# Kernel tuning notes

Measured on AMD Instinct MI355X. Metric: run time of the kernel, lower is better.

The kernel has to match this reference:

```python
import jax, jax.numpy as jnp
import numpy as np
from functools import reduce

N_QUBITS = 12
DIM = 2 ** N_QUBITS          # 4096 state-vector dimension
DEPTH = 6                    # ansatz rotation layers
BATCH = 256
OBSERVE_BITS = (0, 1, 2)     # Pauli-Z expectation on these qubits
INPUT_SCALING = np.pi


def setup_inputs() -> dict:
    key = jax.random.key(0)
    k1, k2 = jax.random.split(key)
    input_tensor = jax.random.uniform(k1, (BATCH, N_QUBITS), dtype=jnp.float32)
    # param_init_range = (-pi/depth, pi/depth)
    thetas = jax.random.normal(k2, (DEPTH, N_QUBITS), dtype=jnp.float32) * (np.pi / DEPTH)
    return {"input_tensor": input_tensor, "thetas": thetas}


def _ry(theta):
    # RY(theta) = [[cos t/2, -sin t/2], [sin t/2, cos t/2]]
    h = theta * 0.5
    c, s = jnp.cos(h), jnp.sin(h)
    return jnp.stack([jnp.stack([c, -s]), jnp.stack([s, c])]).astype(jnp.complex64)


def _cnot_ladder_perm():
    # CNOT(i -> i+1) for i = 0..n-2; each CNOT is a basis permutation that
    # flips the target bit when the control bit is 1. Compose permutations
    # (applied in reverse order so state_out = state_in[perm]). Qubit 0 is the
    # leftmost kron factor, i.e. bit position n-1-q of the basis index.
    perm = np.arange(DIM)
    for cq, tq in reversed([(i, i + 1) for i in range(N_QUBITS - 1)]):
        cbit, tbit = N_QUBITS - 1 - cq, N_QUBITS - 1 - tq
        flip = ((perm >> cbit) & 1) == 1
        perm = np.where(flip, perm ^ (1 << tbit), perm)
    return jnp.asarray(perm)


_PERM = _cnot_ladder_perm()


def _forward(input_tensor, thetas):
    # --- encoder: RY(pi * x_q) applied to |0...0> gives a product state ---
    half = input_tensor * (INPUT_SCALING * 0.5)          # [B, n] half-angles
    c, s = jnp.cos(half), jnp.sin(half)
    psi = jnp.ones((BATCH, 1), dtype=jnp.complex64)
    for q in range(N_QUBITS):                            # fixed small loop over qubits
        amp = jnp.stack([c[:, q], s[:, q]], axis=-1).astype(jnp.complex64)  # [B, 2]
        psi = (psi[:, :, None] * amp[:, None, :]).reshape(BATCH, -1)
    state = psi.T                                        # [DIM, B] complex64

    # --- ansatz: per-depth full-unitary (kron of per-qubit gates) mm, then CNOT ladder ---
    for d in range(DEPTH):
        U = reduce(jnp.kron, [_ry(thetas[d, q]) for q in range(N_QUBITS)])  # [DIM, DIM]
        state = U @ state                                # Hamiltonian @ state (torch.mm)
        state = state[_PERM]                             # entangling CNOT ladder

    # --- observer: <Z_q> on each observed qubit ---
    probs = state.real ** 2 + state.imag ** 2            # [DIM, B]
    idx = jnp.arange(DIM)
    zdiag = jnp.stack([1.0 - 2.0 * ((idx >> (N_QUBITS - 1 - q)) & 1)
                       for q in OBSERVE_BITS]).astype(jnp.float32)          # [K, DIM]
    return jnp.einsum('kn,nb->bk', zdiag, probs)         # [B, K]


def reference(input_tensor, thetas):
    return _forward(input_tensor, thetas)
```

## Files before the change

### kernel.cpp

```cpp
#include <hip/hip_runtime.h>
#include <math.h>
#include <type_traits>

#define NQ     12
#define DIM    4096
#define DEPTH  6
#define NBATCH 256
#define NT     256
#define NREG   16


__host__ __device__ constexpr unsigned axmask(int d, int b) {
    unsigned m = 1u << b;
    for (int i = 0; i < d; ++i) m = (m ^ (m >> 1)) & 0xFFFu;
    return m;
}
__host__ __device__ constexpr unsigned selmask(int d, int b) {
    unsigned m = 1u << b;
    for (int i = 0; i < 16 - d; ++i) m = (m ^ ((m << 1) & 0xFFFu)) & 0xFFFu;
    return m;
}
__host__ __device__ constexpr int cpopc(unsigned v) {
    int c = 0; while (v) { c += (int)(v & 1u); v >>= 1; } return c;
}

template<int I, int N, class F>
__device__ __forceinline__ void sfor(F&& f) {
    if constexpr (I < N) {
        f(std::integral_constant<int, I>{});
        sfor<I + 1, N>(static_cast<F&&>(f));
    }
}

template<int CTRL>
__device__ __forceinline__ float dppx(float v) {
    int iv = __float_as_int(v);
    return __int_as_float(__builtin_amdgcn_update_dpp(iv, iv, CTRL, 0xF, 0xF, false));
}
template<int M4>
__device__ __forceinline__ float lxor_low(float v) {
    static_assert(M4 >= 1 && M4 <= 15, "low mask");
    if constexpr      (M4 == 1)  return dppx<0xB1>(v);
    else if constexpr (M4 == 2)  return dppx<0x4E>(v);
    else if constexpr (M4 == 3)  return dppx<0x1B>(v);
    else if constexpr (M4 == 7)  return dppx<0x141>(v);
    else if constexpr (M4 == 15) return dppx<0x140>(v);
    else if constexpr ((M4 & 8) == 0)
        return lxor_low<M4 ^ 7>(dppx<0x141>(v));
    else
        return lxor_low<M4 ^ 15>(dppx<0x140>(v));
}
template<int MASK>
__device__ __forceinline__ float lxor(float v) {
    static_assert(MASK > 0 && MASK < 64, "lane mask");
    if constexpr (MASK >= 32) {
        return __shfl_xor(v, MASK, 64);
    } else if constexpr (MASK >= 16) {
        return __int_as_float(__builtin_amdgcn_ds_swizzle(__float_as_int(v),
                                                          (MASK << 10) | 0x1F));
    } else {
        return lxor_low<MASK>(v);
    }
}

template<int D, int B>
__device__ __forceinline__ void gate_reg(float (&st)[NREG], int tid, float t) {
    constexpr unsigned V = axmask(D, B), M = selmask(D, B);
    static_assert((V >> 4) == 0 && V != 0, "reg gate");
    constexpr int VR = (int)V;
    constexpr unsigned MR = M & 15u, MT = M >> 4;
    const float tp = (__popc(MT & (unsigned)tid) & 1) ? t : -t;
    const float tn = -tp;
    sfor<0, NREG>([&](auto RC) {
        constexpr int r = RC.value, r2 = r ^ VR;
        if constexpr (r2 > r) {
            constexpr bool p0 = (cpopc(MR & (unsigned)r)  & 1) != 0;
            constexpr bool p1 = (cpopc(MR & (unsigned)r2) & 1) != 0;
            float a0 = st[r];
            st[r]  = fmaf(p0 ? tn : tp, st[r2], st[r]);
            st[r2] = fmaf(p1 ? tn : tp, a0,     st[r2]);
        }
    });
}

template<int D, int B>
__device__ __forceinline__ void gate_lane(float (&st)[NREG], int tid, float t) {
    constexpr unsigned V = axmask(D, B), M = selmask(D, B);
    constexpr int VT = (int)(V >> 4), VR = (int)(V & 15u);
    static_assert(VT > 0 && VT < 64, "intra-wave gate");
    static_assert((M & 15u) == 0, "no reg bits in selector for b>=4");
    const float tp = (__popc((M >> 4) & (unsigned)tid) & 1) ? t : -t;
    if constexpr (VR == 0) {
        sfor<0, NREG>([&](auto RC) {
            constexpr int r = RC.value;
            float p = lxor<VT>(st[r]);
            st[r] = fmaf(tp, p, st[r]);
        });
    } else {
        sfor<0, NREG>([&](auto RC) {
            constexpr int r = RC.value, r2 = r ^ VR;
            if constexpr (r2 > r) {
                float pa = lxor<VT>(st[r2]);
                float pb = lxor<VT>(st[r]);
                st[r]  = fmaf(tp, pa, st[r]);
                st[r2] = fmaf(tp, pb, st[r2]);
            }
        });
    }
}

template<int D>
__device__ __forceinline__ void cross2(float (&st)[NREG], int tid,
                                       float t1, float t2,
                                       float* __restrict__ lds) {
    constexpr unsigned V1 = axmask(D, 11), V2 = axmask(D, 10);
    constexpr unsigned M1 = selmask(D, 11), M2 = selmask(D, 10);
    static_assert((V1 & 15u) == 0 && (V2 & 15u) == 0, "cross axes thread-pure");
    static_assert((M1 & 15u) == 0 && (M2 & 15u) == 0, "cross masks thread-pure");
    constexpr int T1 = (int)(V1 >> 4), T2 = (int)(V2 >> 4);
    static_assert((cpopc(M1 & V2) & 1) == 0, "kC sign identity");

    const float t1p = (__popc((M1 >> 4) & (unsigned)tid) & 1) ? t1 : -t1;
    const float t2p = (__popc((M2 >> 4) & (unsigned)tid) & 1) ? t2 : -t2;
    const float t12 = t1p * t2p;

    float* buf = lds + (D & 1) * DIM;
    const int sw = tid & 3;
    sfor<0, 4>([&](auto KC) {
        constexpr int k = KC.value;
        *reinterpret_cast<float4*>(&buf[tid * 16 + 4 * (k ^ sw)]) =
            make_float4(st[4*k], st[4*k+1], st[4*k+2], st[4*k+3]);
    });
    __syncthreads();
    const int p1 = tid ^ T1, p2 = tid ^ T2, p3 = tid ^ (T1 ^ T2);
    const int b1 = p1 * 16, s1w = p1 & 3;
    const int b2 = p2 * 16, s2w = p2 & 3;
    const int b3 = p3 * 16, s3w = p3 & 3;
    sfor<0, 4>([&](auto KC) {
        constexpr int k = KC.value;
        float4 A  = *reinterpret_cast<const float4*>(&buf[b1 + 4 * (k ^ s1w)]);
        float4 Bv = *reinterpret_cast<const float4*>(&buf[b2 + 4 * (k ^ s2w)]);
        float4 Cv = *reinterpret_cast<const float4*>(&buf[b3 + 4 * (k ^ s3w)]);
        float t;
        t = fmaf(t1p, A.x, st[4*k+0]); t = fmaf(t2p, Bv.x, t); st[4*k+0] = fmaf(t12, Cv.x, t);
        t = fmaf(t1p, A.y, st[4*k+1]); t = fmaf(t2p, Bv.y, t); st[4*k+1] = fmaf(t12, Cv.y, t);
        t = fmaf(t1p, A.z, st[4*k+2]); t = fmaf(t2p, Bv.z, t); st[4*k+2] = fmaf(t12, Cv.z, t);
        t = fmaf(t1p, A.w, st[4*k+3]); t = fmaf(t2p, Bv.w, t); st[4*k+3] = fmaf(t12, Cv.w, t);
    });
}

template<int D>
__device__ __forceinline__ float depth_apply(float (&st)[NREG], int tid,
                                             const float* __restrict__ thetas,
                                             float* __restrict__ lds) {
    float tq[12];
    float scd = 1.0f;
    sfor<0, 12>([&](auto QC) {
        constexpr int q = QC.value;
        float rev = thetas[D * 12 + q] * 0.07957747154594767f;
        float cc  = __builtin_amdgcn_cosf(rev);
        float ss  = __builtin_amdgcn_sinf(rev);
        tq[q] = ss * __builtin_amdgcn_rcpf(cc);
        scd  *= cc;
    });
    cross2<D>(st, tid, tq[0], tq[1], lds);
    sfor<2, 12>([&](auto QC) {
        constexpr int Q = QC.value, B = 11 - Q;
        if constexpr (B >= 4) gate_lane<D, B>(st, tid, tq[Q]);
        else                  gate_reg <D, B>(st, tid, tq[Q]);
    });
    return scd;
}

__global__ __launch_bounds__(NT, 1)
void qnet_kernel(const float* __restrict__ x,
                 const float* __restrict__ thetas,
                 float* __restrict__ out)
{
    __shared__ __align__(16) float lds[2 * DIM];
    __shared__ float red[8];

    const int b   = blockIdx.x;
    const int tid = threadIdx.x;

    const float4* xv = reinterpret_cast<const float4*>(x + b * 12);
    float4 xa = xv[0], xb = xv[1], xc = xv[2];
    float xs[12] = {xa.x, xa.y, xa.z, xa.w, xb.x, xb.y, xb.z, xb.w,
                    xc.x, xc.y, xc.z, xc.w};
    float cq[12], sq[12];
    sfor<0, 12>([&](auto QC) {
        constexpr int q = QC.value;
        float rev = xs[q] * 0.25f;
        sq[q] = __builtin_amdgcn_sinf(rev);
        cq[q] = __builtin_amdgcn_cosf(rev);
    });

    float la = 1.0f;
    sfor<0, 8>([&](auto IC) {
        constexpr int i = IC.value;
        la *= ((tid >> i) & 1) ? sq[7 - i] : cq[7 - i];
    });
    float st[NREG];
    st[0] = la;
    sfor<0, 4>([&](auto IC) {
        constexpr int i = IC.value;
        sfor<0, (1 << i)>([&](auto KC) {
            constexpr int k = KC.value;
            float base = st[k];
            st[k + (1 << i)] = base * sq[11 - i];
            st[k]            = base * cq[11 - i];
        });
    });

    float sc = 1.0f;
    sfor<0, 6>([&](auto DC) {
        sc *= depth_apply<DC.value>(st, tid, thetas, lds);
    });

    float tot = 0.0f;
    sfor<0, NREG>([&](auto RC) {
        constexpr int r = RC.value;
        tot = fmaf(st[r], st[r], tot);
    });
    tot *= sc * sc;

    float v = tot;
    v += lxor<1>(v);
    v += lxor<2>(v);
    v += lxor<4>(v);
    v += lxor<8>(v);
    v += lxor<16>(v);
    float u = lxor<32>(v);
    const int w = tid >> 6;
    if ((tid & 63) == 0) {
        red[w]     = v + u;
        red[4 + w] = v - u;
    }
    __syncthreads();
    if (tid == 0) out[b * 3 + 0] = (red[0] + red[1]) - (red[2] + red[3]);
    if (tid == 1) out[b * 3 + 1] = (red[0] - red[1]) + (red[2] - red[3]);
    if (tid == 2) out[b * 3 + 2] = (red[4] + red[5]) - (red[6] + red[7]);
}

extern "C" void kernel_launch(void* const* d_in, const int* in_sizes, int n_in,
                              void* d_out, int out_size, void* d_ws, size_t ws_size,
                              hipStream_t stream) {
    (void)in_sizes; (void)n_in; (void)out_size; (void)d_ws; (void)ws_size;
    const float* x      = (const float*)d_in[0];
    const float* thetas = (const float*)d_in[1];
    float* out          = (float*)d_out;

    qnet_kernel<<<dim3(NBATCH), dim3(NT), 0, stream>>>(x, thetas, out);
}
```

Baseline: 15.70 us.

## Double threads per batch, halve registers per thread, add cross-wave LDS gate

Each block now uses 512 threads holding 8 amplitudes each instead of 256 threads holding 16, so qubit 9 now crosses waves and needs a new LDS exchange step with an extra barrier per depth. Per-depth tangent and cosine precomputation moves to a one-time shared-memory table computed by the first 72 threads. The final reduction is reworked for 8 waves. The aim is more parallelism and occupancy per CU, at the cost of one more LDS round-trip and barrier per layer.

```diff
diff --git a/kernel.cpp b/kernel.cpp
--- a/kernel.cpp
+++ b/kernel.cpp
@@ -6,8 +6,8 @@
 #define DIM    4096
 #define DEPTH  6
 #define NBATCH 256
-#define NT     256
-#define NREG   16
+#define NT     512
+#define NREG   8
 
 
 __host__ __device__ constexpr unsigned axmask(int d, int b) {
@@ -63,12 +63,16 @@
     }
 }
 
+__device__ __forceinline__ int lad(int t, int k) {
+    return t * 8 + 4 * (k ^ ((t >> 2) & 1));
+}
+
 template<int D, int B>
 __device__ __forceinline__ void gate_reg(float (&st)[NREG], int tid, float t) {
     constexpr unsigned V = axmask(D, B), M = selmask(D, B);
-    static_assert((V >> 4) == 0 && V != 0, "reg gate");
+    static_assert((V >> 3) == 0 && V != 0, "reg gate");
     constexpr int VR = (int)V;
-    constexpr unsigned MR = M & 15u, MT = M >> 4;
+    constexpr unsigned MR = M & 7u, MT = M >> 3;
     const float tp = (__popc(MT & (unsigned)tid) & 1) ? t : -t;
     const float tn = -tp;
     sfor<0, NREG>([&](auto RC) {
@@ -86,10 +90,10 @@
 template<int D, int B>
 __device__ __forceinline__ void gate_lane(float (&st)[NREG], int tid, float t) {
     constexpr unsigned V = axmask(D, B), M = selmask(D, B);
-    constexpr int VT = (int)(V >> 4), VR = (int)(V & 15u);
+    constexpr int VT = (int)(V >> 3), VR = (int)(V & 7u);
     static_assert(VT > 0 && VT < 64, "intra-wave gate");
-    static_assert((M & 15u) == 0, "no reg bits in selector for b>=4");
-    const float tp = (__popc((M >> 4) & (unsigned)tid) & 1) ? t : -t;
+    static_assert((M & 7u) == 0, "no reg bits in selector for b>=3");
+    const float tp = (__popc((M >> 3) & (unsigned)tid) & 1) ? t : -t;
     if constexpr (VR == 0) {
         sfor<0, NREG>([&](auto RC) {
             constexpr int r = RC.value;
@@ -110,37 +114,59 @@
 }
 
 template<int D>
+__device__ __forceinline__ void gate9x(float (&st)[NREG], int tid, float t,
+                                       float* __restrict__ lds9) {
+    constexpr unsigned V = axmask(D, 9), M = selmask(D, 9);
+    static_assert((V & 7u) == 0 && (M & 7u) == 0, "b9 reg-pure-free");
+    constexpr int T = (int)(V >> 3);
+    static_assert(T >= 64 && T < 512, "b9 crosses waves");
+    const float tp = (__popc((M >> 3) & (unsigned)tid) & 1) ? t : -t;
+    float* buf = lds9 + (D & 1) * DIM;
+    sfor<0, 2>([&](auto KC) {
+        constexpr int k = KC.value;
+        *reinterpret_cast<float4*>(&buf[lad(tid, k)]) =
+            make_float4(st[4*k], st[4*k+1], st[4*k+2], st[4*k+3]);
+    });
+    __syncthreads();
+    const int p = tid ^ T;
+    sfor<0, 2>([&](auto KC) {
+        constexpr int k = KC.value;
+        float4 pv = *reinterpret_cast<const float4*>(&buf[lad(p, k)]);
+        st[4*k+0] = fmaf(tp, pv.x, st[4*k+0]);
+        st[4*k+1] = fmaf(tp, pv.y, st[4*k+1]);
+        st[4*k+2] = fmaf(tp, pv.z, st[4*k+2]);
+        st[4*k+3] = fmaf(tp, pv.w, st[4*k+3]);
+    });
+}
+
+template<int D>
 __device__ __forceinline__ void cross2(float (&st)[NREG], int tid,
                                        float t1, float t2,
-                                       float* __restrict__ lds) {
+                                       float* __restrict__ lds2) {
     constexpr unsigned V1 = axmask(D, 11), V2 = axmask(D, 10);
     constexpr unsigned M1 = selmask(D, 11), M2 = selmask(D, 10);
-    static_assert((V1 & 15u) == 0 && (V2 & 15u) == 0, "cross axes thread-pure");
-    static_assert((M1 & 15u) == 0 && (M2 & 15u) == 0, "cross masks thread-pure");
-    constexpr int T1 = (int)(V1 >> 4), T2 = (int)(V2 >> 4);
+    static_assert((V1 & 7u) == 0 && (V2 & 7u) == 0, "cross axes reg-free");
+    static_assert((M1 & 7u) == 0 && (M2 & 7u) == 0, "cross masks reg-free");
+    constexpr int T1 = (int)(V1 >> 3), T2 = (int)(V2 >> 3);
     static_assert((cpopc(M1 & V2) & 1) == 0, "kC sign identity");
 
-    const float t1p = (__popc((M1 >> 4) & (unsigned)tid) & 1) ? t1 : -t1;
-    const float t2p = (__popc((M2 >> 4) & (unsigned)tid) & 1) ? t2 : -t2;
+    const float t1p = (__popc((M1 >> 3) & (unsigned)tid) & 1) ? t1 : -t1;
+    const float t2p = (__popc((M2 >> 3) & (unsigned)tid) & 1) ? t2 : -t2;
     const float t12 = t1p * t2p;
 
-    float* buf = lds + (D & 1) * DIM;
-    const int sw = tid & 3;
-    sfor<0, 4>([&](auto KC) {
+    float* buf = lds2 + (D & 1) * DIM;
+    sfor<0, 2>([&](auto KC) {
         constexpr int k = KC.value;
-        *reinterpret_cast<float4*>(&buf[tid * 16 + 4 * (k ^ sw)]) =
+        *reinterpret_cast<float4*>(&buf[lad(tid, k)]) =
             make_float4(st[4*k], st[4*k+1], st[4*k+2], st[4*k+3]);
     });
     __syncthreads();
     const int p1 = tid ^ T1, p2 = tid ^ T2, p3 = tid ^ (T1 ^ T2);
-    const int b1 = p1 * 16, s1w = p1 & 3;
-    const int b2 = p2 * 16, s2w = p2 & 3;
-    const int b3 = p3 * 16, s3w = p3 & 3;
-    sfor<0, 4>([&](auto KC) {
+    sfor<0, 2>([&](auto KC) {
         constexpr int k = KC.value;
-        float4 A  = *reinterpret_cast<const float4*>(&buf[b1 + 4 * (k ^ s1w)]);
-        float4 Bv = *reinterpret_cast<const float4*>(&buf[b2 + 4 * (k ^ s2w)]);
-        float4 Cv = *reinterpret_cast<const float4*>(&buf[b3 + 4 * (k ^ s3w)]);
+        float4 A  = *reinterpret_cast<const float4*>(&buf[lad(p1, k)]);
+        float4 Bv = *reinterpret_cast<const float4*>(&buf[lad(p2, k)]);
+        float4 Cv = *reinterpret_cast<const float4*>(&buf[lad(p3, k)]);
         float t;
         t = fmaf(t1p, A.x, st[4*k+0]); t = fmaf(t2p, Bv.x, t); st[4*k+0] = fmaf(t12, Cv.x, t);
         t = fmaf(t1p, A.y, st[4*k+1]); t = fmaf(t2p, Bv.y, t); st[4*k+1] = fmaf(t12, Cv.y, t);
@@ -150,38 +176,45 @@
 }
 
 template<int D>
-__device__ __forceinline__ float depth_apply(float (&st)[NREG], int tid,
-                                             const float* __restrict__ thetas,
-                                             float* __restrict__ lds) {
-    float tq[12];
-    float scd = 1.0f;
-    sfor<0, 12>([&](auto QC) {
-        constexpr int q = QC.value;
-        float rev = thetas[D * 12 + q] * 0.07957747154594767f;
-        float cc  = __builtin_amdgcn_cosf(rev);
-        float ss  = __builtin_amdgcn_sinf(rev);
-        tq[q] = ss * __builtin_amdgcn_rcpf(cc);
-        scd  *= cc;
-    });
-    cross2<D>(st, tid, tq[0], tq[1], lds);
-    sfor<2, 12>([&](auto QC) {
+__device__ __forceinline__ void depth_apply(float (&st)[NREG], int tid,
+                                            const float* __restrict__ tsh,
+                                            float* __restrict__ lds2,
+                                            float* __restrict__ lds9) {
+    float4 ta = *reinterpret_cast<const float4*>(&tsh[D * 12 + 0]);
+    float4 tb = *reinterpret_cast<const float4*>(&tsh[D * 12 + 4]);
+    float4 tc = *reinterpret_cast<const float4*>(&tsh[D * 12 + 8]);
+    float tq[12] = {ta.x, ta.y, ta.z, ta.w, tb.x, tb.y, tb.z, tb.w,
+                    tc.x, tc.y, tc.z, tc.w};
+    cross2<D>(st, tid, tq[0], tq[1], lds2);
+    gate9x<D>(st, tid, tq[2], lds9);
+    sfor<3, 12>([&](auto QC) {
         constexpr int Q = QC.value, B = 11 - Q;
-        if constexpr (B >= 4) gate_lane<D, B>(st, tid, tq[Q]);
+        if constexpr (B >= 3) gate_lane<D, B>(st, tid, tq[Q]);
         else                  gate_reg <D, B>(st, tid, tq[Q]);
     });
-    return scd;
-}
-
-__global__ __launch_bounds__(NT, 1)
+}
+
+__global__ __launch_bounds__(NT, 2)
 void qnet_kernel(const float* __restrict__ x,
                  const float* __restrict__ thetas,
                  float* __restrict__ out)
 {
-    __shared__ __align__(16) float lds[2 * DIM];
+    __shared__ __align__(16) float lds2[2 * DIM];
+    __shared__ __align__(16) float lds9[2 * DIM];
+    __shared__ __align__(16) float tsh[80];
+    __shared__ __align__(16) float csh[80];
     __shared__ float red[8];
 
     const int b   = blockIdx.x;
     const int tid = threadIdx.x;
+
+    if (tid < 72) {
+        float rev = thetas[tid] * 0.07957747154594767f;
+        float cc  = __builtin_amdgcn_cosf(rev);
+        float ss  = __builtin_amdgcn_sinf(rev);
+        csh[tid] = cc;
+        tsh[tid] = ss * __builtin_amdgcn_rcpf(cc);
+    }
 
     const float4* xv = reinterpret_cast<const float4*>(x + b * 12);
     float4 xa = xv[0], xb = xv[1], xc = xv[2];
@@ -196,13 +229,13 @@
     });
 
     float la = 1.0f;
-    sfor<0, 8>([&](auto IC) {
+    sfor<0, 9>([&](auto IC) {
         constexpr int i = IC.value;
-        la *= ((tid >> i) & 1) ? sq[7 - i] : cq[7 - i];
+        la *= ((tid >> i) & 1) ? sq[8 - i] : cq[8 - i];
     });
     float st[NREG];
     st[0] = la;
-    sfor<0, 4>([&](auto IC) {
+    sfor<0, 3>([&](auto IC) {
         constexpr int i = IC.value;
         sfor<0, (1 << i)>([&](auto KC) {
             constexpr int k = KC.value;
@@ -212,9 +245,17 @@
         });
     });
 
+    __syncthreads();
+
+    sfor<0, 6>([&](auto DC) {
+        depth_apply<DC.value>(st, tid, tsh, lds2, lds9);
+    });
+
     float sc = 1.0f;
-    sfor<0, 6>([&](auto DC) {
-        sc *= depth_apply<DC.value>(st, tid, thetas, lds);
+    sfor<0, 18>([&](auto IC) {
+        constexpr int i = IC.value;
+        float4 c4 = *reinterpret_cast<const float4*>(&csh[4 * i]);
+        sc *= (c4.x * c4.y) * (c4.z * c4.w);
     });
 
     float tot = 0.0f;
@@ -230,16 +271,21 @@
     v += lxor<4>(v);
     v += lxor<8>(v);
     v += lxor<16>(v);
-    float u = lxor<32>(v);
+    v += lxor<32>(v);
     const int w = tid >> 6;
-    if ((tid & 63) == 0) {
-        red[w]     = v + u;
-        red[4 + w] = v - u;
-    }
+    if ((tid & 63) == 0) red[w] = v;
     __syncthreads();
-    if (tid == 0) out[b * 3 + 0] = (red[0] + red[1]) - (red[2] + red[3]);
-    if (tid == 1) out[b * 3 + 1] = (red[0] - red[1]) + (red[2] - red[3]);
-    if (tid == 2) out[b * 3 + 2] = (red[4] + red[5]) - (red[6] + red[7]);
+    if (tid < 3) {
+        float acc = 0.0f;
+        #pragma unroll
+        for (int ww = 0; ww < 8; ++ww) {
+            int par = (tid == 0) ? ((ww >> 2) & 1)
+                    : (tid == 1) ? ((ww >> 1) & 1)
+                    :              (((ww >> 2) ^ ww) & 1);
+            acc += par ? -red[ww] : red[ww];
+        }
+        out[b * 3 + tid] = acc;
+    }
 }
 
 extern "C" void kernel_launch(void* const* d_in, const int* in_sizes, int n_in,
```

Result: faster. 14.41 us, median of 2 (-8.2%).
